# Kernel tuning notes

Measured on AMD Instinct MI355X. Metric: run time of the kernel, lower is better.

## Reference

```python
import jax, jax.numpy as jnp
import numpy as np

B, N, ND = 32, 512, 8        # batch, graph_size, node_dim
L, H, D = 4, 8, 512          # layers, heads, embed_dim
DK = D // H                  # key_dim = val_dim = 64
F = 2048                     # feed_forward_hidden
EPS = 1e-5


def setup_inputs() -> dict:
    key = jax.random.key(0)
    ks = jax.random.split(key, 16)
    u = lambda k, shape, s: jax.random.uniform(k, shape, jnp.float32, -s, s)
    x = jax.random.normal(ks[0], (B, N, ND), dtype=jnp.float32)
    mask = jax.random.randint(ks[1], (B, N, N), 0, 2).astype(jnp.int32)  # 1 = masked
    return {
        "x": x,
        "mask": mask,
        # init_embed Linear(node_dim, embed_dim)
        "We": u(ks[2], (ND, D), 1.0 / np.sqrt(ND)),
        "be": u(ks[3], (D,), 1.0 / np.sqrt(ND)),
        # per-head projections, stacked over layers; torch init: uniform(-1/sqrt(last_dim), ...)
        "Wq": u(ks[4], (L, H, D, DK), 1.0 / np.sqrt(DK)),
        "Wk": u(ks[5], (L, H, D, DK), 1.0 / np.sqrt(DK)),
        "Wv": u(ks[6], (L, H, D, DK), 1.0 / np.sqrt(DK)),
        "Wo": u(ks[7], (L, H, DK, D), 1.0 / np.sqrt(D)),
        # BatchNorm1d affine params (torch default: weight=1, bias=0)
        "g1": jnp.ones((L, D), jnp.float32), "bt1": jnp.zeros((L, D), jnp.float32),
        "g2": jnp.ones((L, D), jnp.float32), "bt2": jnp.zeros((L, D), jnp.float32),
        # FFN
        "W1": u(ks[8], (L, D, F), 1.0 / np.sqrt(D)),
        "bf1": u(ks[9], (L, F), 1.0 / np.sqrt(D)),
        "W2": u(ks[10], (L, F, D), 1.0 / np.sqrt(F)),
        "bf2": u(ks[11], (L, D), 1.0 / np.sqrt(F)),
    }


def _batch_norm(h, g, b):
    # BatchNorm1d in training mode over flattened (B*N, D), biased variance
    hf = h.reshape(-1, h.shape[-1])
    mu = hf.mean(axis=0)
    var = hf.var(axis=0)
    return (h - mu) * jax.lax.rsqrt(var + EPS) * g + b


def reference(x, mask, We, be, Wq, Wk, Wv, Wo, g1, bt1, W1, bf1, W2, bf2, g2, bt2):
    m = mask.astype(bool)[None]                      # [1,B,N,N], True = masked
    scale = 1.0 / np.sqrt(Wq.shape[-1])
    h = x @ We + be                                  # [B,N,D]
    for l in range(Wq.shape[0]):
        # hand-rolled per-head MHA (q = h, self-attention)
        Q = jnp.einsum('bnd,hdk->hbnk', h, Wq[l])
        K = jnp.einsum('bnd,hdk->hbnk', h, Wk[l])
        V = jnp.einsum('bnd,hdv->hbnv', h, Wv[l])
        scores = jnp.einsum('hbqk,hbnk->hbqn', Q, K) * scale   # [H,B,N,N]
        scores = jnp.where(m, -jnp.inf, scores)
        attn = jax.nn.softmax(scores, axis=-1)
        attn = jnp.where(m, 0.0, attn)               # second mask-zeroing pass
        heads = jnp.einsum('hbqn,hbnv->hbqv', attn, V)
        out = jnp.einsum('hbqv,hvd->bqd', heads, Wo[l])
        h = _batch_norm(h + out, g1[l], bt1[l])      # residual + BN
        ff = jax.nn.relu(h @ W1[l] + bf1[l]) @ W2[l] + bf2[l]
        h = _batch_norm(h + ff, g2[l], bt2[l])       # residual + BN
    return (h, h.mean(axis=1))
```

## Files before the change

kernel.cpp:

```cpp
#include <hip/hip_runtime.h>
#include <hip/hip_fp16.h>
#include <math.h>

#define BN_ROWS 16384
#define DIM 512
#define FF 2048
#define LAYERS 4
#define NSEQ 512
#define BATCH 32

typedef _Float16 f16;
typedef __attribute__((ext_vector_type(8))) _Float16 f16x8;
typedef __attribute__((ext_vector_type(4))) _Float16 f16x4;
typedef __attribute__((ext_vector_type(4))) float f32x4;
typedef unsigned long long u64;

__device__ __forceinline__ f32x4 mfma_f16(f16x8 a, f16x8 b, f32x4 c) {
    return __builtin_amdgcn_mfma_f32_16x16x32_f16(a, b, c, 0, 0, 0);
}
__device__ __forceinline__ void gload_lds16(const f16* g, f16* l) {
    __builtin_amdgcn_global_load_lds(
        (const __attribute__((address_space(1))) unsigned int*)g,
        (__attribute__((address_space(3))) unsigned int*)l, 16, 0, 0);
}

__global__ __launch_bounds__(256)
void pack_qkv(const float* __restrict__ Wq, const float* __restrict__ Wk,
              const float* __restrict__ Wv, f16* __restrict__ oh) {
    size_t i = (size_t)blockIdx.x * 256 + threadIdx.x;
    int d = i & 511;
    size_t rr = i >> 9;
    int row = (int)(rr % 1536);
    int lay = (int)(rr / 1536);
    int which = row >> 9, hh = (row >> 6) & 7, k = row & 63;
    const float* W = which == 0 ? Wq : which == 1 ? Wk : Wv;
    oh[i] = (f16)W[(((size_t)lay * 8 + hh) * 512 + d) * 64 + k];
}

__global__ __launch_bounds__(256)
void transpose_w(const float* __restrict__ in, f16* __restrict__ oh, int R, int C) {
    size_t i = (size_t)blockIdx.x * 256 + threadIdx.x;
    int r = (int)(i % R);
    size_t t = i / R;
    int c = (int)(t % C);
    int lay = (int)(t / C);
    oh[i] = (f16)in[((size_t)lay * R + r) * C + c];
}

__global__ __launch_bounds__(256)
void pack_mask(const int* __restrict__ mask, u64* __restrict__ pm) {
    int wid = (blockIdx.x * 256 + threadIdx.x) >> 6;
    int lane = threadIdx.x & 63;
    for (int i = 0; i < 64; i++) {
        size_t word = (size_t)wid * 64 + i;
        u64 bal = __ballot(mask[word * 64 + lane] != 0);
        if (lane == 0) pm[word] = bal;
    }
}

__global__ __launch_bounds__(512)
void embed_kernel(const float* __restrict__ x, const float* __restrict__ We,
                  const float* __restrict__ be, float* __restrict__ h,
                  f16* __restrict__ hf) {
    int row = blockIdx.x, d = threadIdx.x;
    const float* xr = x + (size_t)row * 8;
    float acc = be[d];
#pragma unroll
    for (int c = 0; c < 8; c++) acc += xr[c] * We[c * DIM + d];
    size_t idx = (size_t)row * DIM + d;
    h[idx] = acc;
    hf[idx] = (f16)acc;
}

template<int OUT>
__global__ __launch_bounds__(256)
void gemm_f16(const f16* __restrict__ A, const f16* __restrict__ Bt,
              const float* __restrict__ bias,
              void* __restrict__ O0, void* __restrict__ O1, void* __restrict__ O2,
              int M, int N, int K) {
    __shared__ f16 As[4096];
    __shared__ f16 Bs[4096];
    const int gx = gridDim.x;
    const int nwg = gx * gridDim.y;
    const int id = blockIdx.y * gx + blockIdx.x;
    const int chunk = nwg >> 3;
    const int sid = (id & 7) * chunk + (id >> 3);
    const int row0 = (sid / gx) * 128, col0 = (sid % gx) * 128;

    const int tid = threadIdx.x, l = tid & 63, w = tid >> 6;
    const int wr = w >> 1, wc = w & 1;
    const int fr = l & 15, fq = l >> 4;
    const int srow = l >> 2, skg = (l & 3) * 8;

    f32x4 acc[4][4] = {};
    const size_t aoff = (size_t)(row0 + w * 32 + srow) * K + skg;
    const size_t boff = (size_t)(col0 + w * 32 + srow) * K + skg;

    for (int k0 = 0; k0 < K; k0 += 32) {
        __syncthreads();
        gload_lds16(A + aoff + k0,           &As[(w * 2 + 0) * 512]);
        gload_lds16(A + aoff + 16 * K + k0,  &As[(w * 2 + 1) * 512]);
        gload_lds16(Bt + boff + k0,          &Bs[(w * 2 + 0) * 512]);
        gload_lds16(Bt + boff + 16 * K + k0, &Bs[(w * 2 + 1) * 512]);
        __syncthreads();
        f16x8 a[4], b[4];
#pragma unroll
        for (int i = 0; i < 4; i++)
            a[i] = *(const f16x8*)&As[(wr * 64 + i * 16 + fr) * 32 + fq * 8];
#pragma unroll
        for (int j = 0; j < 4; j++)
            b[j] = *(const f16x8*)&Bs[(wc * 64 + j * 16 + fr) * 32 + fq * 8];
#pragma unroll
        for (int i = 0; i < 4; i++)
#pragma unroll
            for (int j = 0; j < 4; j++)
                acc[i][j] = mfma_f16(a[i], b[j], acc[i][j]);
    }

    if (OUT == 1) {
        f16* C = (f16*)O0;
#pragma unroll
        for (int j = 0; j < 4; j++) {
            int gcol = col0 + wc * 64 + j * 16 + fr;
            float bv = bias[gcol];
#pragma unroll
            for (int i = 0; i < 4; i++) {
                int gr = row0 + wr * 64 + i * 16 + fq * 4;
#pragma unroll
                for (int r = 0; r < 4; r++)
                    C[(size_t)(gr + r) * N + gcol] = (f16)fmaxf(acc[i][j][r] + bv, 0.f);
            }
        }
    } else if (OUT == 2) {
        f16* Qo = (f16*)O0; f16* Ko = (f16*)O1; f16* Vo = (f16*)O2;
#pragma unroll
        for (int j = 0; j < 4; j++) {
            int gcol = col0 + wc * 64 + j * 16 + fr;
            if (gcol < 1024) {
                f16* dst = gcol < 512 ? Qo : Ko;
                int cc = gcol & 511;
#pragma unroll
                for (int i = 0; i < 4; i++) {
                    int gr = row0 + wr * 64 + i * 16 + fq * 4;
#pragma unroll
                    for (int r = 0; r < 4; r++)
                        dst[(size_t)(gr + r) * 512 + cc] = (f16)acc[i][j][r];
                }
            } else {
                int hh = (gcol - 1024) >> 6, v = gcol & 63;
#pragma unroll
                for (int i = 0; i < 4; i++) {
                    int gr = row0 + wr * 64 + i * 16 + fq * 4;
                    int b = gr >> 9, n = gr & 511;
                    f16x4 sv;
#pragma unroll
                    for (int r = 0; r < 4; r++) sv[r] = (f16)acc[i][j][r];
                    *(f16x4*)&Vo[(((size_t)b * 8 + hh) * 64 + v) * 512 + n] = sv;
                }
            }
        }
    } else {
        float* hres = (float*)O0;
        float* st   = (float*)O1;
#pragma unroll
        for (int j = 0; j < 4; j++) {
            int gcol = col0 + wc * 64 + j * 16 + fr;
            float bv = bias ? bias[gcol] : 0.f;
            float csum = 0.f, csq = 0.f;
#pragma unroll
            for (int i = 0; i < 4; i++) {
                int gr = row0 + wr * 64 + i * 16 + fq * 4;
#pragma unroll
                for (int r = 0; r < 4; r++) {
                    size_t idx = (size_t)(gr + r) * N + gcol;
                    float v = acc[i][j][r] + bv + hres[idx];
                    hres[idx] = v;
                    csum += v; csq += v * v;
                }
            }
            csum += __shfl_down(csum, 32, 64); csum += __shfl_down(csum, 16, 64);
            csq  += __shfl_down(csq,  32, 64); csq  += __shfl_down(csq,  16, 64);
            if (fq == 0) {
                atomicAdd(&st[gcol], csum);
                atomicAdd(&st[gcol + 512], csq);
            }
        }
    }
}

__global__ __launch_bounds__(256)
void attn_flash(const f16* __restrict__ Q, const f16* __restrict__ Kg,
                const f16* __restrict__ Vt, const u64* __restrict__ pmask,
                f16* __restrict__ attf) {
    int id = blockIdx.x;
    int wgid = (id & 7) * 128 + (id >> 3);
    int qc = wgid & 3;
    int gid = wgid >> 2;
    int b = gid & 31, hd = gid >> 5;

    __shared__ f16 Kl[2][4096];
    __shared__ f16 Vl[2][4096];
    __shared__ f16 Plds[4][1024];

    const int tid = threadIdx.x, w = tid >> 6, l = tid & 63;
    const int fr = l & 15, fq = l >> 4;

    const int brow = qc * 128 + w * 32;
    const size_t qbase = ((size_t)b * NSEQ + brow) * DIM + hd * 64;
    f16x8 qa[2][2];
#pragma unroll
    for (int sub = 0; sub < 2; sub++)
#pragma unroll
        for (int ks = 0; ks < 2; ks++)
            qa[sub][ks] = *(const f16x8*)(Q + qbase + (size_t)(sub * 16 + fr) * DIM + ks * 32 + fq * 8);

    const f16* ksrc = Kg + (size_t)b * NSEQ * DIM + hd * 64;
    const f16* vsrc = Vt + ((size_t)b * 8 + hd) * 64 * 512;
    const u64* mrow = pmask + ((size_t)b * NSEQ + brow) * 8;

    const int sr = tid & 63;
    const int sg0 = tid >> 6;
    const int sg1 = sg0 + 4;

    float m[2][4], lsum[2][4];
    f32x4 O[2][4];
#pragma unroll
    for (int s = 0; s < 2; s++)
#pragma unroll
        for (int r = 0; r < 4; r++) {
            m[s][r] = -1e30f; lsum[s][r] = 0.f;
            O[s][r] = (f32x4){0.f, 0.f, 0.f, 0.f};
        }

    char* Pb = (char*)&Plds[w][0];

    {
        gload_lds16(ksrc + (size_t)sr * DIM + sg0 * 8,        &Kl[0][tid * 8]);
        gload_lds16(ksrc + (size_t)sr * DIM + sg1 * 8,        &Kl[0][2048 + tid * 8]);
        gload_lds16(vsrc + (size_t)sr * 512 + sg0 * 8,        &Vl[0][tid * 8]);
        gload_lds16(vsrc + (size_t)sr * 512 + sg1 * 8,        &Vl[0][2048 + tid * 8]);
    }

    for (int c = 0; c < 8; c++) {
        const int buf = c & 1;
        __syncthreads();
        if (c < 7) {
            const int n1 = (c + 1) * 64;
            gload_lds16(ksrc + (size_t)(n1 + sr) * DIM + sg0 * 8, &Kl[buf ^ 1][tid * 8]);
            gload_lds16(ksrc + (size_t)(n1 + sr) * DIM + sg1 * 8, &Kl[buf ^ 1][2048 + tid * 8]);
            gload_lds16(vsrc + (size_t)sr * 512 + n1 + sg0 * 8,   &Vl[buf ^ 1][tid * 8]);
            gload_lds16(vsrc + (size_t)sr * 512 + n1 + sg1 * 8,   &Vl[buf ^ 1][2048 + tid * 8]);
        }

        f16x8 kb[4][2];
#pragma unroll
        for (int nt = 0; nt < 4; nt++)
#pragma unroll
            for (int ks = 0; ks < 2; ks++)
                kb[nt][ks] = *(const f16x8*)&Kl[buf][(ks * 4 + fq) * 512 + (nt * 16 + fr) * 8];

        f32x4 ps[2][4];
#pragma unroll
        for (int sub = 0; sub < 2; sub++)
#pragma unroll
            for (int nt = 0; nt < 4; nt++) {
                f32x4 a = {};
                a = mfma_f16(qa[sub][0], kb[nt][0], a);
                a = mfma_f16(qa[sub][1], kb[nt][1], a);
                ps[sub][nt] = a;
            }
#pragma unroll
        for (int sub = 0; sub < 2; sub++)
#pragma unroll
            for (int rr = 0; rr < 4; rr++) {
                u64 bits = mrow[(size_t)(sub * 16 + fq * 4 + rr) * 8 + c];
#pragma unroll
                for (int nt = 0; nt < 4; nt++) {
                    float s = ps[sub][nt][rr] * 0.125f;
                    ps[sub][nt][rr] = ((bits >> (nt * 16 + fr)) & 1ull) ? -INFINITY : s;
                }
            }

        f16x8 vb[4][2];
#pragma unroll
        for (int vt = 0; vt < 4; vt++)
#pragma unroll
            for (int ks = 0; ks < 2; ks++)
                vb[vt][ks] = *(const f16x8*)&Vl[buf][(ks * 4 + fq) * 512 + (vt * 16 + fr) * 8];

#pragma unroll
        for (int sub = 0; sub < 2; sub++) {
            float cm[4], sc[4], cs[4];
#pragma unroll
            for (int rr = 0; rr < 4; rr++) {
                float v = fmaxf(fmaxf(ps[sub][0][rr], ps[sub][1][rr]),
                                fmaxf(ps[sub][2][rr], ps[sub][3][rr]));
#pragma unroll
                for (int msk = 1; msk < 16; msk <<= 1)
                    v = fmaxf(v, __shfl_xor(v, msk, 64));
                cm[rr] = v;
            }
#pragma unroll
            for (int rr = 0; rr < 4; rr++) {
                float mn = fmaxf(m[sub][rr], cm[rr]);
                sc[rr] = __expf(m[sub][rr] - mn);
                m[sub][rr] = mn;
                cs[rr] = 0.f;
            }
#pragma unroll
            for (int nt = 0; nt < 4; nt++)
#pragma unroll
                for (int rr = 0; rr < 4; rr++) {
                    float p = __expf(ps[sub][nt][rr] - m[sub][rr]);
                    ps[sub][nt][rr] = p;
                    cs[rr] += p;
                }
#pragma unroll
            for (int rr = 0; rr < 4; rr++) {
#pragma unroll
                for (int msk = 1; msk < 16; msk <<= 1)
                    cs[rr] += __shfl_xor(cs[rr], msk, 64);
                lsum[sub][rr] = lsum[sub][rr] * sc[rr] + cs[rr];
            }
#pragma unroll
            for (int vt = 0; vt < 4; vt++)
#pragma unroll
                for (int rr = 0; rr < 4; rr++)
                    O[sub][vt][rr] *= sc[rr];
#pragma unroll
            for (int nt = 0; nt < 4; nt++)
#pragma unroll
                for (int rr = 0; rr < 4; rr++) {
                    int row = fq * 4 + rr;
                    int byte = ((row * 64 + nt * 16 + fr) * 2) ^ ((row & 7) << 4);
                    *(f16*)(Pb + byte) = (f16)ps[sub][nt][rr];
                }
            f16x8 pa[2];
#pragma unroll
            for (int ks = 0; ks < 2; ks++) {
                int byte = ((fr * 64 + ks * 32 + fq * 8) * 2) ^ ((fr & 7) << 4);
                pa[ks] = *(const f16x8*)(Pb + byte);
            }
#pragma unroll
            for (int vt = 0; vt < 4; vt++) {
                O[sub][vt] = mfma_f16(pa[0], vb[vt][0], O[sub][vt]);
                O[sub][vt] = mfma_f16(pa[1], vb[vt][1], O[sub][vt]);
            }
        }
    }
#pragma unroll
    for (int sub = 0; sub < 2; sub++) {
        float inv[4];
#pragma unroll
        for (int rr = 0; rr < 4; rr++) inv[rr] = 1.f / lsum[sub][rr];
#pragma unroll
        for (int vt = 0; vt < 4; vt++)
#pragma unroll
            for (int rr = 0; rr < 4; rr++) {
                float v = O[sub][vt][rr] * inv[rr];
                size_t idx = ((size_t)b * NSEQ + brow + sub * 16 + fq * 4 + rr) * DIM
                             + hd * 64 + vt * 16 + fr;
                attf[idx] = (f16)v;
            }
    }
}

__global__ __launch_bounds__(256)
void bn_apply(float* __restrict__ h, f16* __restrict__ hf,
              const float* __restrict__ sums, const float* __restrict__ g,
              const float* __restrict__ bt, float* __restrict__ outp) {
    size_t i4 = (size_t)blockIdx.x * 256 + threadIdx.x;
    size_t idx = i4 * 4;
    int c = (int)(idx & (DIM - 1));
    float4 hv = *(float4*)&h[idx];
    float4 s4 = *(const float4*)&sums[c];
    float4 q4 = *(const float4*)&sums[DIM + c];
    float4 g4 = *(const float4*)&g[c];
    float4 b4 = *(const float4*)&bt[c];
    float o[4];
    const float invn = 1.f / BN_ROWS;
#pragma unroll
    for (int j = 0; j < 4; j++) {
        float mu = ((const float*)&s4)[j] * invn;
        float var = ((const float*)&q4)[j] * invn - mu * mu;
        o[j] = (((const float*)&hv)[j] - mu) * rsqrtf(var + 1e-5f)
               * ((const float*)&g4)[j] + ((const float*)&b4)[j];
    }
    *(float4*)&h[idx] = *(float4*)o;
    if (outp) *(float4*)&outp[idx] = *(float4*)o;
    f16x4 s;
#pragma unroll
    for (int j = 0; j < 4; j++) s[j] = (f16)o[j];
    *(f16x4*)&hf[idx] = s;
}

__global__ __launch_bounds__(512)
void mean_kernel(const float* __restrict__ src, float* __restrict__ out2) {
    int b = blockIdx.x, seg = blockIdx.y, d = threadIdx.x;
    float acc = 0.f;
    for (int n = seg * 64; n < seg * 64 + 64; n++)
        acc += src[((size_t)b * NSEQ + n) * DIM + d];
    atomicAdd(&out2[b * DIM + d], acc * (1.f / NSEQ));
}

extern "C" void kernel_launch(void* const* d_in, const int* in_sizes, int n_in,
                              void* d_out, int out_size, void* d_ws, size_t ws_size,
                              hipStream_t stream) {
    const float* x   = (const float*)d_in[0];
    const int*   mask= (const int*)d_in[1];
    const float* We  = (const float*)d_in[2];
    const float* be  = (const float*)d_in[3];
    const float* Wq  = (const float*)d_in[4];
    const float* Wk  = (const float*)d_in[5];
    const float* Wv  = (const float*)d_in[6];
    const float* Wo  = (const float*)d_in[7];
    const float* g1  = (const float*)d_in[8];
    const float* bt1 = (const float*)d_in[9];
    const float* g2  = (const float*)d_in[10];
    const float* bt2 = (const float*)d_in[11];
    const float* W1  = (const float*)d_in[12];
    const float* bf1 = (const float*)d_in[13];
    const float* W2  = (const float*)d_in[14];
    const float* bf2 = (const float*)d_in[15];
    float* out = (float*)d_out;

    const size_t MiB = 1ull << 20;
    const size_t M1 = (size_t)BN_ROWS * DIM;
    char* base = (char*)d_ws;
    float* h     = (float*)base;
    f16*   hf    = (f16*)(base + 32 * MiB);
    f16*   Qf    = (f16*)(base + 48 * MiB);
    f16*   Kf    = (f16*)(base + 64 * MiB);
    f16*   Vt    = (f16*)(base + 80 * MiB);
    f16*   attf  = (f16*)(base + 96 * MiB);
    f16*   ffh   = (f16*)(base + 48 * MiB);
    float* stats = (float*)(base + 112 * MiB);
    u64*   pmask = (u64*)(base + 112 * MiB + 65536);
    f16*   wqkv  = (f16*)(base + 114 * MiB);
    f16*   wo    = wqkv + (size_t)4 * 1536 * 512;
    f16*   w1t   = wo   + (size_t)4 * 512 * 512;
    f16*   w2t   = w1t  + (size_t)4 * 2048 * 512;

    pack_qkv<<<dim3(4 * 1536 * 512 / 256), dim3(256), 0, stream>>>(Wq, Wk, Wv, wqkv);
    transpose_w<<<dim3(4 * 512 * 512 / 256), dim3(256), 0, stream>>>(Wo, wo, 512, 512);
    transpose_w<<<dim3(4 * 512 * 2048 / 256), dim3(256), 0, stream>>>(W1, w1t, 512, 2048);
    transpose_w<<<dim3(4 * 2048 * 512 / 256), dim3(256), 0, stream>>>(W2, w2t, 2048, 512);
    pack_mask<<<dim3(512), dim3(256), 0, stream>>>(mask, pmask);
    hipMemsetAsync(out + M1, 0, BATCH * DIM * sizeof(float), stream);

    embed_kernel<<<dim3(BN_ROWS), dim3(512), 0, stream>>>(x, We, be, h, hf);

    for (int l = 0; l < LAYERS; l++) {
        gemm_f16<2><<<dim3(1536 / 128, 128), dim3(256), 0, stream>>>(
            hf, wqkv + (size_t)l * 1536 * 512, nullptr, Qf, Kf, Vt,
            BN_ROWS, 1536, 512);

        attn_flash<<<dim3(1024), dim3(256), 0, stream>>>(Qf, Kf, Vt, pmask, attf);

        hipMemsetAsync(stats, 0, 1024 * sizeof(float), stream);
        gemm_f16<3><<<dim3(512 / 128, 128), dim3(256), 0, stream>>>(
            attf, wo + (size_t)l * 512 * 512, nullptr, h, stats, nullptr,
            BN_ROWS, 512, 512);
        bn_apply<<<dim3(M1 / 1024), dim3(256), 0, stream>>>(
            h, hf, stats, g1 + l * DIM, bt1 + l * DIM, nullptr);

        hipMemsetAsync(stats, 0, 1024 * sizeof(float), stream);
        gemm_f16<1><<<dim3(FF / 128, BN_ROWS / 128), dim3(256), 0, stream>>>(
            hf, w1t + (size_t)l * FF * DIM, bf1 + (size_t)l * FF,
            ffh, nullptr, nullptr, BN_ROWS, FF, DIM);
        gemm_f16<3><<<dim3(DIM / 128, BN_ROWS / 128), dim3(256), 0, stream>>>(
            ffh, w2t + (size_t)l * DIM * FF, bf2 + (size_t)l * DIM,
            h, stats, nullptr, BN_ROWS, DIM, FF);

        float* outp = (l == LAYERS - 1) ? out : nullptr;
        bn_apply<<<dim3(M1 / 1024), dim3(256), 0, stream>>>(
            h, hf, stats, g2 + l * DIM, bt2 + l * DIM, outp);
    }

    mean_kernel<<<dim3(BATCH, 8), dim3(512), 0, stream>>>(out, out + M1);
}
```

Before: 1.303 ms.

## Use lazy max rescaling, exp2 scores, and MFMA row sums in attention softmax

Softmax scores are pre-scaled by log2(e)/sqrt(dk) so exp2 can replace exp. The running max is only updated, with its shuffle reduction and rescale of O and the sum, when some row's chunk max exceeds the stored max by a threshold, checked wave-wide with __any. Row sums are computed by an extra MFMA against a vector of ones instead of shuffle reductions. This removes most cross-lane shuffles per chunk, but adds two MFMAs per sub-tile. Probabilities can reach up to 2^11 before the f16 cast and the fp16 accumulation of the row sum, which risks some precision loss.

After: 1.260 ms. -3.3%, faster.

```diff
diff --git a/kernel.cpp b/kernel.cpp
--- a/kernel.cpp
+++ b/kernel.cpp
@@ -222,24 +222,27 @@
     const int sg0 = tid >> 6;
     const int sg1 = sg0 + 4;
 
-    float m[2][4], lsum[2][4];
-    f32x4 O[2][4];
+    const float SC = 0.18033688011112042f;
+    const float THR = 11.0f;
+
+    float mu[2][4];
+    f32x4 O[2][4] = {};
+    f32x4 S1[2] = {};
 #pragma unroll
     for (int s = 0; s < 2; s++)
 #pragma unroll
-        for (int r = 0; r < 4; r++) {
-            m[s][r] = -1e30f; lsum[s][r] = 0.f;
-            O[s][r] = (f32x4){0.f, 0.f, 0.f, 0.f};
-        }
+        for (int r = 0; r < 4; r++) mu[s][r] = -1e30f;
+
+    f16x8 vones;
+#pragma unroll
+    for (int i = 0; i < 8; i++) vones[i] = (f16)1.0f;
 
     char* Pb = (char*)&Plds[w][0];
 
-    {
-        gload_lds16(ksrc + (size_t)sr * DIM + sg0 * 8,        &Kl[0][tid * 8]);
-        gload_lds16(ksrc + (size_t)sr * DIM + sg1 * 8,        &Kl[0][2048 + tid * 8]);
-        gload_lds16(vsrc + (size_t)sr * 512 + sg0 * 8,        &Vl[0][tid * 8]);
-        gload_lds16(vsrc + (size_t)sr * 512 + sg1 * 8,        &Vl[0][2048 + tid * 8]);
-    }
+    gload_lds16(ksrc + (size_t)sr * DIM + sg0 * 8, &Kl[0][tid * 8]);
+    gload_lds16(ksrc + (size_t)sr * DIM + sg1 * 8, &Kl[0][2048 + tid * 8]);
+    gload_lds16(vsrc + (size_t)sr * 512 + sg0 * 8, &Vl[0][tid * 8]);
+    gload_lds16(vsrc + (size_t)sr * 512 + sg1 * 8, &Vl[0][2048 + tid * 8]);
 
     for (int c = 0; c < 8; c++) {
         const int buf = c & 1;
@@ -276,8 +279,8 @@
                 u64 bits = mrow[(size_t)(sub * 16 + fq * 4 + rr) * 8 + c];
 #pragma unroll
                 for (int nt = 0; nt < 4; nt++) {
-                    float s = ps[sub][nt][rr] * 0.125f;
-                    ps[sub][nt][rr] = ((bits >> (nt * 16 + fr)) & 1ull) ? -INFINITY : s;
+                    float u = ps[sub][nt][rr] * SC;
+                    ps[sub][nt][rr] = ((bits >> (nt * 16 + fr)) & 1ull) ? -INFINITY : u;
                 }
             }
 
@@ -290,43 +293,34 @@
 
 #pragma unroll
         for (int sub = 0; sub < 2; sub++) {
-            float cm[4], sc[4], cs[4];
-#pragma unroll
-            for (int rr = 0; rr < 4; rr++) {
-                float v = fmaxf(fmaxf(ps[sub][0][rr], ps[sub][1][rr]),
-                                fmaxf(ps[sub][2][rr], ps[sub][3][rr]));
-#pragma unroll
-                for (int msk = 1; msk < 16; msk <<= 1)
-                    v = fmaxf(v, __shfl_xor(v, msk, 64));
-                cm[rr] = v;
-            }
-#pragma unroll
-            for (int rr = 0; rr < 4; rr++) {
-                float mn = fmaxf(m[sub][rr], cm[rr]);
-                sc[rr] = __expf(m[sub][rr] - mn);
-                m[sub][rr] = mn;
-                cs[rr] = 0.f;
+            float lmax[4];
+#pragma unroll
+            for (int rr = 0; rr < 4; rr++)
+                lmax[rr] = fmaxf(fmaxf(ps[sub][0][rr], ps[sub][1][rr]),
+                                 fmaxf(ps[sub][2][rr], ps[sub][3][rr]));
+            bool over = (lmax[0] > mu[sub][0] + THR) | (lmax[1] > mu[sub][1] + THR) |
+                        (lmax[2] > mu[sub][2] + THR) | (lmax[3] > mu[sub][3] + THR);
+            if (__any(over)) {
+#pragma unroll
+                for (int rr = 0; rr < 4; rr++) {
+                    float v = lmax[rr];
+#pragma unroll
+                    for (int msk = 1; msk < 16; msk <<= 1)
+                        v = fmaxf(v, __shfl_xor(v, msk, 64));
+                    float mn = fmaxf(mu[sub][rr], v);
+                    float sc = exp2f(mu[sub][rr] - mn);
+                    mu[sub][rr] = mn;
+                    S1[sub][rr] *= sc;
+#pragma unroll
+                    for (int vt = 0; vt < 4; vt++)
+                        O[sub][vt][rr] *= sc;
+                }
             }
 #pragma unroll
             for (int nt = 0; nt < 4; nt++)
 #pragma unroll
-                for (int rr = 0; rr < 4; rr++) {
-                    float p = __expf(ps[sub][nt][rr] - m[sub][rr]);
-                    ps[sub][nt][rr] = p;
-                    cs[rr] += p;
-                }
-#pragma unroll
-            for (int rr = 0; rr < 4; rr++) {
-#pragma unroll
-                for (int msk = 1; msk < 16; msk <<= 1)
-                    cs[rr] += __shfl_xor(cs[rr], msk, 64);
-                lsum[sub][rr] = lsum[sub][rr] * sc[rr] + cs[rr];
-            }
-#pragma unroll
-            for (int vt = 0; vt < 4; vt++)
-#pragma unroll
                 for (int rr = 0; rr < 4; rr++)
-                    O[sub][vt][rr] *= sc[rr];
+                    ps[sub][nt][rr] = exp2f(ps[sub][nt][rr] - mu[sub][rr]);
 #pragma unroll
             for (int nt = 0; nt < 4; nt++)
 #pragma unroll
@@ -341,6 +335,8 @@
                 int byte = ((fr * 64 + ks * 32 + fq * 8) * 2) ^ ((fr & 7) << 4);
                 pa[ks] = *(const f16x8*)(Pb + byte);
             }
+            S1[sub] = mfma_f16(pa[0], vones, S1[sub]);
+            S1[sub] = mfma_f16(pa[1], vones, S1[sub]);
 #pragma unroll
             for (int vt = 0; vt < 4; vt++) {
                 O[sub][vt] = mfma_f16(pa[0], vb[vt][0], O[sub][vt]);
@@ -352,7 +348,7 @@
     for (int sub = 0; sub < 2; sub++) {
         float inv[4];
 #pragma unroll
-        for (int rr = 0; rr < 4; rr++) inv[rr] = 1.f / lsum[sub][rr];
+        for (int rr = 0; rr < 4; rr++) inv[rr] = 1.f / S1[sub][rr];
 #pragma unroll
         for (int vt = 0; vt < 4; vt++)
 #pragma unroll
```
